# Optimization experiments

Measured on AMD Instinct MI355X. Metric: run time of the kernel, lower is better.

## Reference

```python
import jax, jax.numpy as jnp
import numpy as np

D, P, S, E = 200, 200, 150, 150  # drugs, proteins, diseases, side-effects
EMB = 256

def setup_inputs() -> dict:
    key = jax.random.key(0)
    ks = jax.random.split(key, 10)
    s = 0.05
    type_mask = jnp.concatenate([
        jnp.zeros(D, jnp.int64) if False else jnp.full((D,), 0, jnp.int32),
        jnp.full((P,), 1, jnp.int32),
        jnp.full((S,), 2, jnp.int32),
        jnp.full((E,), 3, jnp.int32)]).astype(jnp.int32)
    return {
        'type_mask': type_mask,
        'entity_embedding': jax.random.normal(ks[0], (D + P + S + E, EMB)) * s,
        'relation_embedding': jax.random.normal(ks[1], (1200, EMB)) * s,
        'W_ent': jax.random.normal(ks[2], (EMB, EMB)) * s,
        'W_rel': jax.random.normal(ks[3], (EMB, EMB)) * s,
        'W1': jax.random.normal(ks[4], (2 * EMB, 1024)) * s,
        'b1': jnp.zeros((1024,)),
        'W2': jax.random.normal(ks[5], (1024, 512)) * s,
        'b2': jnp.zeros((512,)),
        'W3': jax.random.normal(ks[6], (512, 2)) * s,
        'b3': jnp.zeros((2,)),
    }

def _pair_softmax(a, b, W1, b1, W2, b2, W3, b3):
    # classifier(concat(a[i], b[j])) for the full cartesian product.
    # First linear is decomposed: W1 @ [a;b] = a@W1a + b@W1b (same math,
    # avoids materializing the [Na*Nb, 2*EMB] concat tensor).
    W1a, W1b = W1[:EMB], W1[EMB:]
    ha = a @ W1a                      # [Na, 1024]
    hb = b @ W1b                      # [Nb, 1024]
    h = jax.nn.relu(ha[:, None, :] + hb[None, :, :] + b1)  # [Na, Nb, 1024]
    h = jax.nn.relu(h @ W2 + b2)      # [Na, Nb, 512]
    logits = h @ W3 + b3              # [Na, Nb, 2]
    Na, Nb = a.shape[0], b.shape[0]
    return jax.nn.softmax(logits.reshape(Na * Nb, 2), axis=-1)

def reference(type_mask, entity_embedding, relation_embedding, W_ent, W_rel,
              W1, b1, W2, b2, W3, b3):
    tm = np.asarray(type_mask)  # concrete, block-structured type ids
    idx = [np.nonzero(tm == t)[0] for t in range(4)]
    # project embeddings (project_on path; nn.Linear: x @ W)
    ent = entity_embedding @ W_ent
    _rel = relation_embedding @ W_rel  # computed in original forward, unused (graph_on off)
    drug, prot, dis, se = (ent[idx[0]], ent[idx[1]], ent[idx[2]], ent[idx[3]])
    cls = lambda a, b: _pair_softmax(a, b, W1, b1, W2, b2, W3, b3)
    out_dp = cls(drug, prot)
    out_dd = cls(drug, drug)
    out_ds = cls(drug, dis)
    out_de = cls(drug, se)
    out_ps = cls(prot, dis)
    out_pp = cls(prot, prot)
    out_pd = cls(prot, drug)
    out_ed = cls(se, drug)
    out_sp = cls(dis, prot)
    out_sd = cls(dis, drug)
    return (out_dp, out_dd, out_ds, out_de, out_ps, out_pp, out_pd,
            out_ed, out_sp, out_sd, drug)
```

## Files before the change

### kernel.cpp

```cpp
#include <hip/hip_runtime.h>
#include <hip/hip_bf16.h>

typedef __attribute__((ext_vector_type(4))) float floatx4;
typedef __attribute__((ext_vector_type(8))) __bf16 bf16x8;
typedef unsigned short ushort_t;

#define NENT  700
#define EMB   256
#define KDIM  1024
#define NDIM  512
#define HROWS 720
#define NPAIR 340000

#define WS_HA   0
#define WS_HB   (WS_HA + HROWS*KDIM*2)
#define WS_W2H  (WS_HB + HROWS*KDIM*2)
#define WS_ENT  (WS_W2H + NDIM*KDIM*2)
#define WS_LG   (WS_ENT + NENT*EMB*4)

__device__ __forceinline__ float ldin(const void* p, int i, int isbf) {
    return isbf ? __bfloat162float(((const __hip_bfloat16*)p)[i])
                : ((const float*)p)[i];
}

__device__ __forceinline__ int detect_bf16(const ushort_t* __restrict__ w) {
    int t = threadIdx.x & 63;
    int e = (w[2*t] >> 7) & 0xFF;
    unsigned long long m = __ballot(e >= 100 && e <= 126);
    return (__popcll(m) >= 48) ? 1 : 0;
}

#define LDS_BARRIER() do { __builtin_amdgcn_s_waitcnt(0xC07F); __builtin_amdgcn_s_barrier(); } while (0)

__global__ void entprep_kernel(const void* __restrict__ E, const void* __restrict__ Went,
                               const void* __restrict__ W2,
                               float* __restrict__ ent, __hip_bfloat16* __restrict__ W2H,
                               void* __restrict__ out) {
    int isbf = detect_bf16((const ushort_t*)E);
    if (blockIdx.x < 88) {
        int ib = blockIdx.x * 8, t = threadIdx.x;
        __shared__ float rows[8][EMB];
#pragma unroll
        for (int r = 0; r < 8; ++r) {
            int i = ib + r;
            rows[r][t] = (i < NENT) ? ldin(E, i*EMB + t, isbf) : 0.f;
        }
        __syncthreads();
        float acc[8] = {0.f,0.f,0.f,0.f,0.f,0.f,0.f,0.f};
        if (isbf) {
            const __hip_bfloat16* W = (const __hip_bfloat16*)Went;
            for (int k = 0; k < EMB; ++k) {
                float w = __bfloat162float(W[k*EMB + t]);
#pragma unroll
                for (int r = 0; r < 8; ++r) acc[r] += rows[r][k] * w;
            }
        } else {
            const float* W = (const float*)Went;
            for (int k = 0; k < EMB; ++k) {
                float w = W[k*EMB + t];
#pragma unroll
                for (int r = 0; r < 8; ++r) acc[r] += rows[r][k] * w;
            }
        }
#pragma unroll
        for (int r = 0; r < 8; ++r) {
            int i = ib + r;
            if (i < NENT) {
                ent[i*EMB + t] = acc[r];
                if (i < 200) {
                    if (isbf) ((__hip_bfloat16*)out)[680000 + i*EMB + t] = __float2bfloat16(acc[r]);
                    else      ((float*)out)[680000 + i*EMB + t] = acc[r];
                }
            }
        }
    } else {
        int g = (blockIdx.x - 88)*256 + threadIdx.x;
        int lane = g & 63, f = (g >> 6) & 15, kc = (g >> 10) & 31, half = g >> 15;
        int l15 = lane & 15, quad = lane >> 4;
        int n = half*256 + f*16 + l15;
        bf16x8 v;
#pragma unroll
        for (int j = 0; j < 8; ++j) {
            int k = kc*32 + quad*8 + j;
            v[j] = (__bf16)ldin(W2, k*NDIM + n, isbf);
        }
        *(bf16x8*)(W2H + (size_t)g*8) = v;
    }
}

__global__ void hab_kernel(const float* __restrict__ ent, const void* __restrict__ E,
                           const void* __restrict__ W1, const void* __restrict__ b1,
                           __hip_bfloat16* __restrict__ HA, __hip_bfloat16* __restrict__ HB) {
    int isbf = detect_bf16((const ushort_t*)E);
    int part = blockIdx.y;
    int ib = blockIdx.x * 16;
    int t = threadIdx.x;
    __shared__ float rows[16][EMB];
#pragma unroll
    for (int r = 0; r < 16; ++r) {
        int i = ib + r;
        rows[r][t] = (i < NENT) ? ent[i*EMB + t] : 0.f;
    }
    __syncthreads();
    float acc[16][4];
#pragma unroll
    for (int r = 0; r < 16; ++r)
#pragma unroll
        for (int p = 0; p < 4; ++p) acc[r][p] = 0.f;

    int wbase = part*EMB*KDIM;
    if (isbf) {
        const __hip_bfloat16* W = (const __hip_bfloat16*)W1;
        for (int k = 0; k < EMB; ++k) {
            float w[4];
#pragma unroll
            for (int p = 0; p < 4; ++p) w[p] = __bfloat162float(W[wbase + k*KDIM + t + p*256]);
#pragma unroll
            for (int r = 0; r < 16; ++r) {
                float e = rows[r][k];
#pragma unroll
                for (int p = 0; p < 4; ++p) acc[r][p] += e * w[p];
            }
        }
    } else {
        const float* W = (const float*)W1;
        for (int k = 0; k < EMB; ++k) {
            float w[4];
#pragma unroll
            for (int p = 0; p < 4; ++p) w[p] = W[wbase + k*KDIM + t + p*256];
#pragma unroll
            for (int r = 0; r < 16; ++r) {
                float e = rows[r][k];
#pragma unroll
                for (int p = 0; p < 4; ++p) acc[r][p] += e * w[p];
            }
        }
    }
    __hip_bfloat16* HX = part ? HB : HA;
#pragma unroll
    for (int r = 0; r < 16; ++r) {
#pragma unroll
        for (int p = 0; p < 4; ++p) {
            int n = t + p*256;
            float v = acc[r][p];
            if (!part) v += ldin(b1, n, isbf);
            HX[(ib + r)*KDIM + n] = __float2bfloat16(v);
        }
    }
}

union U8 { bf16x8 v; unsigned u[4]; };

__device__ __forceinline__ bf16x8 mk_af3(bf16x8 ha, bf16x8 hb) {
    U8 r;
#pragma unroll
    for (int j = 0; j < 4; ++j) {
        float x0 = fmaxf((float)ha[2*j]   + (float)hb[2*j],   0.f);
        float x1 = fmaxf((float)ha[2*j+1] + (float)hb[2*j+1], 0.f);
        unsigned u0 = __float_as_uint(x0) + 0x8000u;
        unsigned u1 = __float_as_uint(x1) + 0x8000u;
#if defined(__has_builtin) && __has_builtin(__builtin_amdgcn_perm)
        r.u[j] = __builtin_amdgcn_perm(u1, u0, 0x07060302u);
#else
        r.u[j] = (u0 >> 16) | (u1 & 0xFFFF0000u);
#endif
    }
    return r.v;
}

#define MFMA(a, b, c) __builtin_amdgcn_mfma_f32_16x16x32_bf16((a), (b), (c), 0, 0, 0)

__global__ __launch_bounds__(256, 3) void pair_kernel(
        const ushort_t* __restrict__ HA, const ushort_t* __restrict__ HB,
        const ushort_t* __restrict__ W2H, const void* __restrict__ E,
        const void* __restrict__ b2, const void* __restrict__ W3,
        float* __restrict__ Lg, void* __restrict__ out) {

    const int blkEnd[10] = {650,1300,1800,2300,2800,3450,4100,4594,5088,5582};
    const int aB[10]  = {0,0,0,0,200,200,200,550,400,400};
    const int bB[10]  = {200,0,400,550,400,200,0,0,200,0};
    const int NaT[10] = {200,200,200,200,200,200,200,150,150,150};
    const int NbT[10] = {200,200,150,150,150,200,200,200,200,200};
    const int jTl[10] = {13,13,10,10,10,13,13,13,13,13};
    const int oOf[10] = {0,80000,160000,220000,280000,340000,420000,500000,560000,620000};

    __shared__ __align__(16) unsigned char sAF[16384];
    __shared__ float lgt[4][64][2];

    int bid = blockIdx.x;
    int half = blockIdx.y;
    int ty = 0;
    while (bid >= blkEnd[ty]) ty++;
    int lb = bid - (ty ? blkEnd[ty-1] : 0);
    int jT = jTl[ty];
    int it = lb / jT;
    int jt = lb - it*jT;
    int i0 = aB[ty] + it*4;
    int j0 = bB[ty] + jt*16;

    int tid  = threadIdx.x;
    int lane = tid & 63;
    int w    = tid >> 6;
    int l15  = lane & 15;
    int quad = lane >> 4;
    int kb   = (bid*7 + half*3) & 31;

    const char* WB = (const char*)W2H + ((size_t)((half*32)*16 + w*4))*1024 + lane*16;
    const ushort_t* HBp = HB + (j0 + l15)*KDIM + quad*8;
    const ushort_t* HAp = HA + (i0 + w)*KDIM + quad*8;

    floatx4 acc[4][4];
#pragma unroll
    for (int mf = 0; mf < 4; ++mf)
#pragma unroll
        for (int nf = 0; nf < 4; ++nf) acc[mf][nf] = (floatx4){0.f,0.f,0.f,0.f};

    {
        int k0 = kb, k1 = (kb + 1) & 31;
        bf16x8 Bc0p = *(const bf16x8*)(WB + (size_t)k0*16384);
        (void)Bc0p;
    }
    int k0 = kb, k1 = (kb + 1) & 31;
    bf16x8 Bc0 = *(const bf16x8*)(WB + (size_t)k0*16384);
    bf16x8 Bc1 = *(const bf16x8*)(WB + (size_t)k0*16384 + 1024);
    bf16x8 Bc2 = *(const bf16x8*)(WB + (size_t)k0*16384 + 2048);
    bf16x8 Bc3 = *(const bf16x8*)(WB + (size_t)k0*16384 + 3072);
    bf16x8 Bn0 = *(const bf16x8*)(WB + (size_t)k1*16384);
    bf16x8 Bn1 = *(const bf16x8*)(WB + (size_t)k1*16384 + 1024);
    bf16x8 Bn2 = *(const bf16x8*)(WB + (size_t)k1*16384 + 2048);
    bf16x8 Bn3 = *(const bf16x8*)(WB + (size_t)k1*16384 + 3072);
    bf16x8 haA = *(const bf16x8*)(HAp + k0*32);
    bf16x8 haB = *(const bf16x8*)(HAp + k1*32);
    bf16x8 hbA = *(const bf16x8*)(HBp + k0*32);
    bf16x8 hbB = *(const bf16x8*)(HBp + k1*32);

#pragma unroll 2
    for (int ph = 0; ph < 16; ++ph) {
        int kn2 = (2*ph + 2 + kb) & 31;
        int kn3 = (2*ph + 3 + kb) & 31;
        bf16x8 nhaA = *(const bf16x8*)(HAp + kn2*32);
        bf16x8 nhaB = *(const bf16x8*)(HAp + kn3*32);
        bf16x8 nhbA = *(const bf16x8*)(HBp + kn2*32);
        bf16x8 nhbB = *(const bf16x8*)(HBp + kn3*32);

        char* sW = (char*)sAF + (ph & 1)*8192 + w*1024 + lane*16;
        *(bf16x8*)(sW)        = mk_af3(haA, hbA);
        *(bf16x8*)(sW + 4096) = mk_af3(haB, hbB);
        LDS_BARRIER();

        const char* sR = (const char*)sAF + (ph & 1)*8192 + lane*16;
        {
            bf16x8 a0 = *(const bf16x8*)(sR);
            bf16x8 a1 = *(const bf16x8*)(sR + 1024);
            bf16x8 a2 = *(const bf16x8*)(sR + 2048);
            bf16x8 a3 = *(const bf16x8*)(sR + 3072);
            acc[0][0] = MFMA(a0, Bc0, acc[0][0]); acc[1][0] = MFMA(a1, Bc0, acc[1][0]);
            acc[2][0] = MFMA(a2, Bc0, acc[2][0]); acc[3][0] = MFMA(a3, Bc0, acc[3][0]);
            acc[0][1] = MFMA(a0, Bc1, acc[0][1]); acc[1][1] = MFMA(a1, Bc1, acc[1][1]);
            acc[2][1] = MFMA(a2, Bc1, acc[2][1]); acc[3][1] = MFMA(a3, Bc1, acc[3][1]);
            acc[0][2] = MFMA(a0, Bc2, acc[0][2]); acc[1][2] = MFMA(a1, Bc2, acc[1][2]);
            acc[2][2] = MFMA(a2, Bc2, acc[2][2]); acc[3][2] = MFMA(a3, Bc2, acc[3][2]);
            acc[0][3] = MFMA(a0, Bc3, acc[0][3]); acc[1][3] = MFMA(a1, Bc3, acc[1][3]);
            acc[2][3] = MFMA(a2, Bc3, acc[2][3]); acc[3][3] = MFMA(a3, Bc3, acc[3][3]);
        }
        Bc0 = *(const bf16x8*)(WB + (size_t)kn2*16384);
        Bc1 = *(const bf16x8*)(WB + (size_t)kn2*16384 + 1024);
        Bc2 = *(const bf16x8*)(WB + (size_t)kn2*16384 + 2048);
        Bc3 = *(const bf16x8*)(WB + (size_t)kn2*16384 + 3072);
        {
            bf16x8 a0 = *(const bf16x8*)(sR + 4096);
            bf16x8 a1 = *(const bf16x8*)(sR + 4096 + 1024);
            bf16x8 a2 = *(const bf16x8*)(sR + 4096 + 2048);
            bf16x8 a3 = *(const bf16x8*)(sR + 4096 + 3072);
            acc[0][0] = MFMA(a0, Bn0, acc[0][0]); acc[1][0] = MFMA(a1, Bn0, acc[1][0]);
            acc[2][0] = MFMA(a2, Bn0, acc[2][0]); acc[3][0] = MFMA(a3, Bn0, acc[3][0]);
            acc[0][1] = MFMA(a0, Bn1, acc[0][1]); acc[1][1] = MFMA(a1, Bn1, acc[1][1]);
            acc[2][1] = MFMA(a2, Bn1, acc[2][1]); acc[3][1] = MFMA(a3, Bn1, acc[3][1]);
            acc[0][2] = MFMA(a0, Bn2, acc[0][2]); acc[1][2] = MFMA(a1, Bn2, acc[1][2]);
            acc[2][2] = MFMA(a2, Bn2, acc[2][2]); acc[3][2] = MFMA(a3, Bn2, acc[3][2]);
            acc[0][3] = MFMA(a0, Bn3, acc[0][3]); acc[1][3] = MFMA(a1, Bn3, acc[1][3]);
            acc[2][3] = MFMA(a2, Bn3, acc[2][3]); acc[3][3] = MFMA(a3, Bn3, acc[3][3]);
        }
        Bn0 = *(const bf16x8*)(WB + (size_t)kn3*16384);
        Bn1 = *(const bf16x8*)(WB + (size_t)kn3*16384 + 1024);
        Bn2 = *(const bf16x8*)(WB + (size_t)kn3*16384 + 2048);
        Bn3 = *(const bf16x8*)(WB + (size_t)kn3*16384 + 3072);

        haA = nhaA; haB = nhaB; hbA = nhbA; hbB = nhbB;
    }

    int isbf = detect_bf16((const ushort_t*)E);
    int nb = half*256 + w*64;
    float b2v[4], wa[4], wb[4];
#pragma unroll
    for (int nf = 0; nf < 4; ++nf) {
        int n = nb + nf*16 + l15;
        b2v[nf] = ldin(b2, n, isbf);
        wa[nf]  = ldin(W3, 2*n, isbf);
        wb[nf]  = ldin(W3, 2*n+1, isbf);
    }
#pragma unroll
    for (int mf = 0; mf < 4; ++mf) {
        float s0[4] = {0.f,0.f,0.f,0.f};
        float s1[4] = {0.f,0.f,0.f,0.f};
#pragma unroll
        for (int nf = 0; nf < 4; ++nf) {
            floatx4 c = acc[mf][nf];
#pragma unroll
            for (int r = 0; r < 4; ++r) {
                float v = fmaxf(c[r] + b2v[nf], 0.f);
                s0[r] += v * wa[nf];
                s1[r] += v * wb[nf];
            }
        }
#pragma unroll
        for (int off = 1; off < 16; off <<= 1) {
#pragma unroll
            for (int r = 0; r < 4; ++r) {
                s0[r] += __shfl_xor(s0[r], off, 64);
                s1[r] += __shfl_xor(s1[r], off, 64);
            }
        }
        if (l15 == 0) {
#pragma unroll
            for (int r = 0; r < 4; ++r) {
                int p = mf*16 + quad*4 + r;
                lgt[w][p][0] = s0[r];
                lgt[w][p][1] = s1[r];
            }
        }
    }
    __syncthreads();

    if (tid < 64) {
        int p = tid;
        float l0 = lgt[0][p][0] + lgt[1][p][0] + lgt[2][p][0] + lgt[3][p][0];
        float l1 = lgt[0][p][1] + lgt[1][p][1] + lgt[2][p][1] + lgt[3][p][1];
        int pi = it*4 + (p >> 4), pj = jt*16 + (p & 15);
        if (pi < NaT[ty] && pj < NbT[ty]) {
            int o = oOf[ty] + (pi*NbT[ty] + pj)*2;
            if (half == 0) {
                if (isbf) {
                    __hip_bfloat16* ob = (__hip_bfloat16*)out;
                    ob[o] = __float2bfloat16(l0); ob[o+1] = __float2bfloat16(l1);
                } else {
                    float* of = (float*)out;
                    of[o] = l0; of[o+1] = l1;
                }
            } else {
                Lg[o] = l0; Lg[o+1] = l1;
            }
        }
    }
}

__global__ void final_kernel(const float* __restrict__ Lg, const void* __restrict__ b3,
                             const void* __restrict__ E, void* __restrict__ out) {
    int isbf = detect_bf16((const ushort_t*)E);
    int g = blockIdx.x*512 + threadIdx.x;
    if (g >= NPAIR) return;
    float h0, h1;
    if (isbf) {
        h0 = __bfloat162float(((const __hip_bfloat16*)out)[2*g]);
        h1 = __bfloat162float(((const __hip_bfloat16*)out)[2*g+1]);
    } else {
        h0 = ((const float*)out)[2*g];
        h1 = ((const float*)out)[2*g+1];
    }
    float l0 = h0 + Lg[2*g]   + ldin(b3, 0, isbf);
    float l1 = h1 + Lg[2*g+1] + ldin(b3, 1, isbf);
    float mx = fmaxf(l0, l1);
    float e0 = __expf(l0 - mx), e1 = __expf(l1 - mx);
    float inv = 1.f / (e0 + e1);
    if (isbf) {
        __hip_bfloat16* ob = (__hip_bfloat16*)out;
        ob[2*g]   = __float2bfloat16(e0 * inv);
        ob[2*g+1] = __float2bfloat16(e1 * inv);
    } else {
        float* of = (float*)out;
        of[2*g]   = e0 * inv;
        of[2*g+1] = e1 * inv;
    }
}

extern "C" void kernel_launch(void* const* d_in, const int* in_sizes, int n_in,
                              void* d_out, int out_size, void* d_ws, size_t ws_size,
                              hipStream_t stream) {
    const void* E    = d_in[1];
    const void* Went = d_in[3];
    const void* W1   = d_in[5];
    const void* b1   = d_in[6];
    const void* W2   = d_in[7];
    const void* b2   = d_in[8];
    const void* W3   = d_in[9];
    const void* b3   = d_in[10];

    char* ws = (char*)d_ws;
    __hip_bfloat16* HA   = (__hip_bfloat16*)(ws + WS_HA);
    __hip_bfloat16* HB   = (__hip_bfloat16*)(ws + WS_HB);
    __hip_bfloat16* W2H  = (__hip_bfloat16*)(ws + WS_W2H);
    float*          entf = (float*)(ws + WS_ENT);
    float*          Lg   = (float*)(ws + WS_LG);

    entprep_kernel<<<dim3(344), dim3(256), 0, stream>>>(E, Went, W2, entf, W2H, d_out);
    hab_kernel<<<dim3(45, 2), dim3(256), 0, stream>>>(entf, E, W1, b1, HA, HB);
    pair_kernel<<<dim3(5582, 2), dim3(256), 0, stream>>>((const ushort_t*)HA, (const ushort_t*)HB,
                                                         (const ushort_t*)W2H, E, b2, W3, Lg, d_out);
    final_kernel<<<dim3((NPAIR + 511)/512), dim3(512), 0, stream>>>(Lg, b3, E, d_out);
}
```

Measured before the change: 566.6 us.

## Build A fragments per wave in registers instead of sharing through LDS

Before, each wave built the relu(ha+hb) fragment for its own A row, wrote it to shared memory and hit a block barrier every step so all four waves could read every row. Now each wave loads all four HA rows plus its HB slice straight from global memory and builds all four fragments in registers. This removes the LDS traffic and the per-step barriers. In exchange it does four times as many mk_af3 VALU conversions and HA loads per wave, and drops to single-step prefetch, which could raise register pressure and VALU load.

```diff
diff --git a/kernel.cpp b/kernel.cpp
--- a/kernel.cpp
+++ b/kernel.cpp
@@ -29,8 +29,6 @@
     unsigned long long m = __ballot(e >= 100 && e <= 126);
     return (__popcll(m) >= 48) ? 1 : 0;
 }
-
-#define LDS_BARRIER() do { __builtin_amdgcn_s_waitcnt(0xC07F); __builtin_amdgcn_s_barrier(); } while (0)
 
 __global__ void entprep_kernel(const void* __restrict__ E, const void* __restrict__ Went,
                                const void* __restrict__ W2,
@@ -184,7 +182,6 @@
     const int jTl[10] = {13,13,10,10,10,13,13,13,13,13};
     const int oOf[10] = {0,80000,160000,220000,280000,340000,420000,500000,560000,620000};
 
-    __shared__ __align__(16) unsigned char sAF[16384];
     __shared__ float lgt[4][64][2];
 
     int bid = blockIdx.x;
@@ -207,7 +204,7 @@
 
     const char* WB = (const char*)W2H + ((size_t)((half*32)*16 + w*4))*1024 + lane*16;
     const ushort_t* HBp = HB + (j0 + l15)*KDIM + quad*8;
-    const ushort_t* HAp = HA + (i0 + w)*KDIM + quad*8;
+    const ushort_t* HAp = HA + i0*KDIM + quad*8;
 
     floatx4 acc[4][4];
 #pragma unroll
@@ -215,78 +212,46 @@
 #pragma unroll
         for (int nf = 0; nf < 4; ++nf) acc[mf][nf] = (floatx4){0.f,0.f,0.f,0.f};
 
+    bf16x8 Bc0 = *(const bf16x8*)(WB + (size_t)kb*16384);
+    bf16x8 Bc1 = *(const bf16x8*)(WB + (size_t)kb*16384 + 1024);
+    bf16x8 Bc2 = *(const bf16x8*)(WB + (size_t)kb*16384 + 2048);
+    bf16x8 Bc3 = *(const bf16x8*)(WB + (size_t)kb*16384 + 3072);
+    bf16x8 af0, af1, af2, af3;
     {
-        int k0 = kb, k1 = (kb + 1) & 31;
-        bf16x8 Bc0p = *(const bf16x8*)(WB + (size_t)k0*16384);
-        (void)Bc0p;
-    }
-    int k0 = kb, k1 = (kb + 1) & 31;
-    bf16x8 Bc0 = *(const bf16x8*)(WB + (size_t)k0*16384);
-    bf16x8 Bc1 = *(const bf16x8*)(WB + (size_t)k0*16384 + 1024);
-    bf16x8 Bc2 = *(const bf16x8*)(WB + (size_t)k0*16384 + 2048);
-    bf16x8 Bc3 = *(const bf16x8*)(WB + (size_t)k0*16384 + 3072);
-    bf16x8 Bn0 = *(const bf16x8*)(WB + (size_t)k1*16384);
-    bf16x8 Bn1 = *(const bf16x8*)(WB + (size_t)k1*16384 + 1024);
-    bf16x8 Bn2 = *(const bf16x8*)(WB + (size_t)k1*16384 + 2048);
-    bf16x8 Bn3 = *(const bf16x8*)(WB + (size_t)k1*16384 + 3072);
-    bf16x8 haA = *(const bf16x8*)(HAp + k0*32);
-    bf16x8 haB = *(const bf16x8*)(HAp + k1*32);
-    bf16x8 hbA = *(const bf16x8*)(HBp + k0*32);
-    bf16x8 hbB = *(const bf16x8*)(HBp + k1*32);
+        bf16x8 hb0 = *(const bf16x8*)(HBp + kb*32);
+        bf16x8 h0 = *(const bf16x8*)(HAp + kb*32);
+        bf16x8 h1 = *(const bf16x8*)(HAp + KDIM + kb*32);
+        bf16x8 h2 = *(const bf16x8*)(HAp + 2*KDIM + kb*32);
+        bf16x8 h3 = *(const bf16x8*)(HAp + 3*KDIM + kb*32);
+        af0 = mk_af3(h0, hb0); af1 = mk_af3(h1, hb0);
+        af2 = mk_af3(h2, hb0); af3 = mk_af3(h3, hb0);
+    }
 
 #pragma unroll 2
-    for (int ph = 0; ph < 16; ++ph) {
-        int kn2 = (2*ph + 2 + kb) & 31;
-        int kn3 = (2*ph + 3 + kb) & 31;
-        bf16x8 nhaA = *(const bf16x8*)(HAp + kn2*32);
-        bf16x8 nhaB = *(const bf16x8*)(HAp + kn3*32);
-        bf16x8 nhbA = *(const bf16x8*)(HBp + kn2*32);
-        bf16x8 nhbB = *(const bf16x8*)(HBp + kn3*32);
-
-        char* sW = (char*)sAF + (ph & 1)*8192 + w*1024 + lane*16;
-        *(bf16x8*)(sW)        = mk_af3(haA, hbA);
-        *(bf16x8*)(sW + 4096) = mk_af3(haB, hbB);
-        LDS_BARRIER();
-
-        const char* sR = (const char*)sAF + (ph & 1)*8192 + lane*16;
-        {
-            bf16x8 a0 = *(const bf16x8*)(sR);
-            bf16x8 a1 = *(const bf16x8*)(sR + 1024);
-            bf16x8 a2 = *(const bf16x8*)(sR + 2048);
-            bf16x8 a3 = *(const bf16x8*)(sR + 3072);
-            acc[0][0] = MFMA(a0, Bc0, acc[0][0]); acc[1][0] = MFMA(a1, Bc0, acc[1][0]);
-            acc[2][0] = MFMA(a2, Bc0, acc[2][0]); acc[3][0] = MFMA(a3, Bc0, acc[3][0]);
-            acc[0][1] = MFMA(a0, Bc1, acc[0][1]); acc[1][1] = MFMA(a1, Bc1, acc[1][1]);
-            acc[2][1] = MFMA(a2, Bc1, acc[2][1]); acc[3][1] = MFMA(a3, Bc1, acc[3][1]);
-            acc[0][2] = MFMA(a0, Bc2, acc[0][2]); acc[1][2] = MFMA(a1, Bc2, acc[1][2]);
-            acc[2][2] = MFMA(a2, Bc2, acc[2][2]); acc[3][2] = MFMA(a3, Bc2, acc[3][2]);
-            acc[0][3] = MFMA(a0, Bc3, acc[0][3]); acc[1][3] = MFMA(a1, Bc3, acc[1][3]);
-            acc[2][3] = MFMA(a2, Bc3, acc[2][3]); acc[3][3] = MFMA(a3, Bc3, acc[3][3]);
-        }
-        Bc0 = *(const bf16x8*)(WB + (size_t)kn2*16384);
-        Bc1 = *(const bf16x8*)(WB + (size_t)kn2*16384 + 1024);
-        Bc2 = *(const bf16x8*)(WB + (size_t)kn2*16384 + 2048);
-        Bc3 = *(const bf16x8*)(WB + (size_t)kn2*16384 + 3072);
-        {
-            bf16x8 a0 = *(const bf16x8*)(sR + 4096);
-            bf16x8 a1 = *(const bf16x8*)(sR + 4096 + 1024);
-            bf16x8 a2 = *(const bf16x8*)(sR + 4096 + 2048);
-            bf16x8 a3 = *(const bf16x8*)(sR + 4096 + 3072);
-            acc[0][0] = MFMA(a0, Bn0, acc[0][0]); acc[1][0] = MFMA(a1, Bn0, acc[1][0]);
-            acc[2][0] = MFMA(a2, Bn0, acc[2][0]); acc[3][0] = MFMA(a3, Bn0, acc[3][0]);
-            acc[0][1] = MFMA(a0, Bn1, acc[0][1]); acc[1][1] = MFMA(a1, Bn1, acc[1][1]);
-            acc[2][1] = MFMA(a2, Bn1, acc[2][1]); acc[3][1] = MFMA(a3, Bn1, acc[3][1]);
-            acc[0][2] = MFMA(a0, Bn2, acc[0][2]); acc[1][2] = MFMA(a1, Bn2, acc[1][2]);
-            acc[2][2] = MFMA(a2, Bn2, acc[2][2]); acc[3][2] = MFMA(a3, Bn2, acc[3][2]);
-            acc[0][3] = MFMA(a0, Bn3, acc[0][3]); acc[1][3] = MFMA(a1, Bn3, acc[1][3]);
-            acc[2][3] = MFMA(a2, Bn3, acc[2][3]); acc[3][3] = MFMA(a3, Bn3, acc[3][3]);
-        }
-        Bn0 = *(const bf16x8*)(WB + (size_t)kn3*16384);
-        Bn1 = *(const bf16x8*)(WB + (size_t)kn3*16384 + 1024);
-        Bn2 = *(const bf16x8*)(WB + (size_t)kn3*16384 + 2048);
-        Bn3 = *(const bf16x8*)(WB + (size_t)kn3*16384 + 3072);
-
-        haA = nhaA; haB = nhaB; hbA = nhbA; hbB = nhbB;
+    for (int kc = 0; kc < 32; ++kc) {
+        int kn = (kc + 1 + kb) & 31;
+        bf16x8 Bn0 = *(const bf16x8*)(WB + (size_t)kn*16384);
+        bf16x8 Bn1 = *(const bf16x8*)(WB + (size_t)kn*16384 + 1024);
+        bf16x8 Bn2 = *(const bf16x8*)(WB + (size_t)kn*16384 + 2048);
+        bf16x8 Bn3 = *(const bf16x8*)(WB + (size_t)kn*16384 + 3072);
+        bf16x8 hbn = *(const bf16x8*)(HBp + kn*32);
+        bf16x8 hn0 = *(const bf16x8*)(HAp + kn*32);
+        bf16x8 hn1 = *(const bf16x8*)(HAp + KDIM + kn*32);
+        bf16x8 hn2 = *(const bf16x8*)(HAp + 2*KDIM + kn*32);
+        bf16x8 hn3 = *(const bf16x8*)(HAp + 3*KDIM + kn*32);
+
+        acc[0][0] = MFMA(af0, Bc0, acc[0][0]); acc[1][0] = MFMA(af1, Bc0, acc[1][0]);
+        acc[2][0] = MFMA(af2, Bc0, acc[2][0]); acc[3][0] = MFMA(af3, Bc0, acc[3][0]);
+        acc[0][1] = MFMA(af0, Bc1, acc[0][1]); acc[1][1] = MFMA(af1, Bc1, acc[1][1]);
+        acc[2][1] = MFMA(af2, Bc1, acc[2][1]); acc[3][1] = MFMA(af3, Bc1, acc[3][1]);
+        acc[0][2] = MFMA(af0, Bc2, acc[0][2]); acc[1][2] = MFMA(af1, Bc2, acc[1][2]);
+        acc[2][2] = MFMA(af2, Bc2, acc[2][2]); acc[3][2] = MFMA(af3, Bc2, acc[3][2]);
+        acc[0][3] = MFMA(af0, Bc3, acc[0][3]); acc[1][3] = MFMA(af1, Bc3, acc[1][3]);
+        acc[2][3] = MFMA(af2, Bc3, acc[2][3]); acc[3][3] = MFMA(af3, Bc3, acc[3][3]);
+
+        af0 = mk_af3(hn0, hbn); af1 = mk_af3(hn1, hbn);
+        af2 = mk_af3(hn2, hbn); af3 = mk_af3(hn3, hbn);
+        Bc0 = Bn0; Bc1 = Bn1; Bc2 = Bn2; Bc3 = Bn3;
     }
 
     int isbf = detect_bf16((const ushort_t*)E);
```

New measurement: 907.8 us. 60.2% more time.
